# Kernel optimization log

Measured on AMD Instinct MI355X. Metric: run time of the kernel, lower is better.

The kernel has to match this reference:

```python
import jax, jax.numpy as jnp
import numpy as np
from jax import lax

WINDOW_SIZE = 11
SIGMA = 1.5
CHANNEL = 1
C1 = 0.01 ** 2
C2 = 0.03 ** 2
EPS = 1e-8


def _gaussian_window(window_size, sigma, channel):
    coords = jnp.arange(window_size, dtype=jnp.float32) - window_size // 2
    g = jnp.exp(-coords ** 2 / (2.0 * sigma ** 2))
    g = g / g.sum()
    w2d = jnp.outer(g, g)  # [ws, ws]
    # depthwise conv kernel, OIHW with I=1 (groups=channel)
    return jnp.broadcast_to(w2d[None, None], (channel, 1, window_size, window_size))


def _blur(x, window, channel):
    # depthwise 2D conv, SAME padding (padding = ws//2 for odd ws)
    return lax.conv_general_dilated(
        x, window, window_strides=(1, 1), padding="SAME",
        feature_group_count=channel,
        dimension_numbers=("NCHW", "OIHW", "NCHW"))


def setup_inputs() -> dict:
    key = jax.random.key(0)
    k1, k2 = jax.random.split(key)
    B, C, H, W = 32, CHANNEL, 512, 512
    pred = jax.random.uniform(k1, (B, C, H, W), dtype=jnp.float32)
    target = jax.random.uniform(k2, (B, C, H, W), dtype=jnp.float32)
    window = _gaussian_window(WINDOW_SIZE, SIGMA, CHANNEL)
    return {"pred": pred, "target": target, "window": window}


def reference(pred, target, window):
    channel = pred.shape[1]
    mu_p = _blur(pred, window, channel)
    mu_t = _blur(target, window, channel)
    mu_p_sq = mu_p ** 2
    mu_t_sq = mu_t ** 2
    mu_pt = mu_p * mu_t
    sigma_p_sq = _blur(pred ** 2, window, channel) - mu_p_sq
    sigma_t_sq = _blur(target ** 2, window, channel) - mu_t_sq
    sigma_pt = _blur(pred * target, window, channel) - mu_pt
    sigma_p_sq = jnp.maximum(sigma_p_sq, 0.0)
    sigma_t_sq = jnp.maximum(sigma_t_sq, 0.0)
    numerator = (2.0 * mu_pt + C1) * (2.0 * sigma_pt + C2)
    denominator = (mu_p_sq + mu_t_sq + C1) * (sigma_p_sq + sigma_t_sq + C2)
    ssim_map = numerator / (denominator + EPS)
    return 1.0 - jnp.mean(ssim_map)
```

## Files before the change

kernel.cpp:

```cpp
#include <hip/hip_runtime.h>

typedef short  s16x8 __attribute__((ext_vector_type(8)));
typedef unsigned short u16x8 __attribute__((ext_vector_type(8)));
typedef float  f32x4 __attribute__((ext_vector_type(4)));

#define B_   32
#define H_   512
#define W_   512
#define TX_  64
#define TY_  32
#define RX_  80
#define RYP_ 48
#define VXP_ 88
#define NBLK (B_ * (W_/TX_) * (H_/TY_))

__device__ __forceinline__ unsigned short f2bf(float x) {
    unsigned u = __builtin_bit_cast(unsigned, x);
    u += 0x7FFFu + ((u >> 16) & 1u);
    return (unsigned short)(u >> 16);
}

__global__ __launch_bounds__(256, 3)
void ssim_main(const float* __restrict__ pred,
               const float* __restrict__ targ,
               const float* __restrict__ win,
               float* __restrict__ partial)
{
    __shared__ __align__(16) unsigned short rawT[4][RX_][RYP_];
    __shared__ __align__(16) unsigned short vbuf[4][TY_][VXP_];
    __shared__ float gw[16];
    __shared__ float wsum[4];

    const int tid  = threadIdx.x;
    const int lane = tid & 63;
    const int wv   = tid >> 6;
    const int bid  = blockIdx.x;
    const int b    = bid >> 7;
    const int rem  = bid & 127;
    const int ty   = rem >> 3;
    const int tx   = rem & 7;
    const int x0g  = tx * TX_ - 5;
    const int y0g  = ty * TY_ - 5;

    if (tid < 11) {
        float s = 0.f;
        #pragma unroll
        for (int j = 0; j < 11; ++j) s += win[tid*11 + j];
        gw[tid] = s;
    }

    const float* pb = pred + (size_t)b * (H_*W_);
    const float* tb = targ + (size_t)b * (H_*W_);

    for (int idx = tid; idx < RX_ * 24; idx += 256) {
        const int x_l = idx % RX_;
        const int rp  = idx / RX_;
        const int gx  = x0g + x_l;
        const int gy0 = y0g + 2*rp;
        const bool xv = (unsigned)gx < (unsigned)W_;
        float p0=0.f, t0=0.f, p1=0.f, t1=0.f;
        if (xv && (unsigned)gy0 < (unsigned)H_) {
            const size_t o = (size_t)gy0 * W_ + gx; p0 = pb[o]; t0 = tb[o];
        }
        if (xv && (unsigned)(gy0+1) < (unsigned)H_) {
            const size_t o = (size_t)(gy0+1) * W_ + gx; p1 = pb[o]; t1 = tb[o];
        }
        const float s0 = fmaf(p0,p0, t0*t0), s1 = fmaf(p1,p1, t1*t1);
        const float q0 = p0*t0,              q1 = p1*t1;
        const int yo = 2*rp;
        *(unsigned*)&rawT[0][x_l][yo] = (unsigned)f2bf(p0) | ((unsigned)f2bf(p1) << 16);
        *(unsigned*)&rawT[1][x_l][yo] = (unsigned)f2bf(t0) | ((unsigned)f2bf(t1) << 16);
        *(unsigned*)&rawT[2][x_l][yo] = (unsigned)f2bf(s0) | ((unsigned)f2bf(s1) << 16);
        *(unsigned*)&rawT[3][x_l][yo] = (unsigned)f2bf(q0) | ((unsigned)f2bf(q1) << 16);
    }
    __syncthreads();

    const int mrow = lane & 15;
    const int quad = lane >> 4;
    s16x8 afr;
    #pragma unroll
    for (int j = 0; j < 8; ++j) {
        const int d = quad*8 + j - mrow;
        const float f = (d >= 0 && d < 11) ? gw[d] : 0.f;
        afr[j] = (short)f2bf(f);
    }
    const f32x4 zero4 = {0.f, 0.f, 0.f, 0.f};

    #pragma unroll
    for (int it = 0; it < 10; ++it) {
        const int X0c = (it >> 1) * 16;
        const int Yt  = (it & 1) * 16;
        const int xcol = X0c + mrow;
        const u16x8 braw = *(const u16x8*)&rawT[wv][xcol][Yt + quad*8];
        const s16x8 bfr  = __builtin_bit_cast(s16x8, braw);
        const f32x4 d = __builtin_amdgcn_mfma_f32_16x16x32_bf16(afr, bfr, zero4, 0, 0, 0);
        #pragma unroll
        for (int r = 0; r < 4; ++r)
            vbuf[wv][Yt + quad*4 + r][xcol] = f2bf(d[r]);
    }
    __syncthreads();

    float lsum = 0.f;
    const int X0 = wv * 16;
    #pragma unroll
    for (int yt = 0; yt < 2; ++yt) {
        const int Y0c = yt * 16;
        f32x4 dq[4];
        #pragma unroll
        for (int pl = 0; pl < 4; ++pl) {
            const u16x8 bv = *(const u16x8*)&vbuf[pl][Y0c + mrow][X0 + quad*8];
            const s16x8 bfr = __builtin_bit_cast(s16x8, bv);
            dq[pl] = __builtin_amdgcn_mfma_f32_16x16x32_bf16(afr, bfr, zero4, 0, 0, 0);
        }
        #pragma unroll
        for (int r = 0; r < 4; ++r) {
            const float mp = dq[0][r], mt = dq[1][r];
            const float sv = dq[2][r], qv = dq[3][r];
            const float mp2 = mp*mp, mt2 = mt*mt, mpt = mp*mt;
            const float sig = fmaxf(sv - mp2 - mt2, 0.f);
            const float cv  = qv - mpt;
            const float num = (2.f*mpt + 1e-4f) * (2.f*cv + 9e-4f);
            const float den = (mp2 + mt2 + 1e-4f) * (sig + 9e-4f);
            lsum += num * __builtin_amdgcn_rcpf(den + 1e-8f);
        }
    }

    #pragma unroll
    for (int off = 32; off > 0; off >>= 1)
        lsum += __shfl_down(lsum, off, 64);
    if (lane == 0) wsum[wv] = lsum;
    __syncthreads();
    if (tid == 0)
        partial[bid] = wsum[0] + wsum[1] + wsum[2] + wsum[3];
}

__global__ __launch_bounds__(256)
void ssim_reduce(const float* __restrict__ partial, float* __restrict__ out)
{
    __shared__ double ws[4];
    double s = 0.0;
    for (int i = threadIdx.x; i < NBLK; i += 256) s += (double)partial[i];
    #pragma unroll
    for (int off = 32; off > 0; off >>= 1)
        s += __shfl_down(s, off, 64);
    if ((threadIdx.x & 63) == 0) ws[threadIdx.x >> 6] = s;
    __syncthreads();
    if (threadIdx.x == 0) {
        const double tot = ws[0] + ws[1] + ws[2] + ws[3];
        const double n = (double)B_ * (double)H_ * (double)W_;
        out[0] = (float)(1.0 - tot / n);
    }
}

extern "C" void kernel_launch(void* const* d_in, const int* in_sizes, int n_in,
                              void* d_out, int out_size, void* d_ws, size_t ws_size,
                              hipStream_t stream)
{
    const float* pred = (const float*)d_in[0];
    const float* targ = (const float*)d_in[1];
    const float* win  = (const float*)d_in[2];
    float* out     = (float*)d_out;
    float* partial = (float*)d_ws;

    ssim_main<<<NBLK, 256, 0, stream>>>(pred, targ, win, partial);
    ssim_reduce<<<1, 256, 0, stream>>>(partial, out);
}
```

Before: 125.3 us.

## Fuse reduction into main kernel, use fp16 MFMA and smaller tiles

Reduces the output tile to 64x16 to double the block count and raise the occupancy target. Switches bf16 MFMA to fp16 with hardware packed conversion, and adds an XOR-swizzled LDS layout. Adds a branch-free interior load path. Replaces the separate reduction kernel with a last-block-done atomic counter to remove one launch. The trade-off is more halo reloading per output pixel and a persistent counter stored in the workspace.

```diff
diff --git a/kernel.cpp b/kernel.cpp
--- a/kernel.cpp
+++ b/kernel.cpp
@@ -1,125 +1,139 @@
 #include <hip/hip_runtime.h>
 
-typedef short  s16x8 __attribute__((ext_vector_type(8)));
-typedef unsigned short u16x8 __attribute__((ext_vector_type(8)));
-typedef float  f32x4 __attribute__((ext_vector_type(4)));
+typedef _Float16 f16x2 __attribute__((ext_vector_type(2)));
+typedef _Float16 f16x4 __attribute__((ext_vector_type(4)));
+typedef _Float16 f16x8 __attribute__((ext_vector_type(8)));
+typedef float    f32x4 __attribute__((ext_vector_type(4)));
 
-#define B_   32
-#define H_   512
-#define W_   512
-#define TX_  64
-#define TY_  32
-#define RX_  80
-#define RYP_ 48
-#define VXP_ 88
-#define NBLK (B_ * (W_/TX_) * (H_/TY_))
+#define NBLK 8192
 
-__device__ __forceinline__ unsigned short f2bf(float x) {
-    unsigned u = __builtin_bit_cast(unsigned, x);
-    u += 0x7FFFu + ((u >> 16) & 1u);
-    return (unsigned short)(u >> 16);
+__device__ __forceinline__ f16x2 pkrtz(float a, float b) {
+    return __builtin_bit_cast(f16x2, __builtin_amdgcn_cvt_pkrtz(a, b));
 }
 
-__global__ __launch_bounds__(256, 3)
-void ssim_main(const float* __restrict__ pred,
-               const float* __restrict__ targ,
-               const float* __restrict__ win,
-               float* __restrict__ partial)
+__global__ __launch_bounds__(256, 5)
+void ssim_fused(const float* __restrict__ pred,
+                const float* __restrict__ targ,
+                const float* __restrict__ win,
+                float* __restrict__ partial,
+                unsigned int* __restrict__ cnt,
+                float* __restrict__ out)
 {
-    __shared__ __align__(16) unsigned short rawT[4][RX_][RYP_];
-    __shared__ __align__(16) unsigned short vbuf[4][TY_][VXP_];
-    __shared__ float gw[16];
-    __shared__ float wsum[4];
+    __shared__ __align__(16) _Float16 rawT[4 * 80 * 32];
+    __shared__ __align__(16) _Float16 vbuf[4 * 16 * 88];
+    __shared__ float  gw[16];
+    __shared__ float  wsum[4];
+    __shared__ double dsum[4];
+    __shared__ int    go;
 
     const int tid  = threadIdx.x;
     const int lane = tid & 63;
     const int wv   = tid >> 6;
     const int bid  = blockIdx.x;
-    const int b    = bid >> 7;
-    const int rem  = bid & 127;
+    const int b    = bid >> 8;
+    const int rem  = bid & 255;
     const int ty   = rem >> 3;
     const int tx   = rem & 7;
-    const int x0g  = tx * TX_ - 5;
-    const int y0g  = ty * TY_ - 5;
+    const int x0g  = tx * 64 - 5;
+    const int y0g  = ty * 16 - 5;
 
     if (tid < 11) {
         float s = 0.f;
         #pragma unroll
-        for (int j = 0; j < 11; ++j) s += win[tid*11 + j];
+        for (int j = 0; j < 11; ++j) s += win[tid * 11 + j];
         gw[tid] = s;
     }
 
-    const float* pb = pred + (size_t)b * (H_*W_);
-    const float* tb = targ + (size_t)b * (H_*W_);
+    const float* pb = pred + (size_t)b * (512 * 512);
+    const float* tb = targ + (size_t)b * (512 * 512);
+    const bool interior = (tx >= 1) & (tx <= 6) & (ty >= 1) & (ty <= 30);
 
-    for (int idx = tid; idx < RX_ * 24; idx += 256) {
-        const int x_l = idx % RX_;
-        const int rp  = idx / RX_;
-        const int gx  = x0g + x_l;
-        const int gy0 = y0g + 2*rp;
-        const bool xv = (unsigned)gx < (unsigned)W_;
-        float p0=0.f, t0=0.f, p1=0.f, t1=0.f;
-        if (xv && (unsigned)gy0 < (unsigned)H_) {
-            const size_t o = (size_t)gy0 * W_ + gx; p0 = pb[o]; t0 = tb[o];
+    if (tid < 240) {
+        const int x  = tid % 80;
+        const int r0 = tid / 80;
+        const int gx = x0g + x;
+        const int sw = (x >> 1) & 7;
+        const bool xok = (unsigned)gx < 512u;
+        _Float16* rb = &rawT[x * 32];
+        for (int qy = r0; qy < 8; qy += 3) {
+            const int gy = y0g + qy * 4;
+            float p0, p1, p2, p3, t0, t1, t2, t3;
+            if (interior) {
+                const float* pp = pb + (size_t)gy * 512 + gx;
+                const float* tp = tb + (size_t)gy * 512 + gx;
+                p0 = pp[0]; p1 = pp[512]; p2 = pp[1024]; p3 = pp[1536];
+                t0 = tp[0]; t1 = tp[512]; t2 = tp[1024]; t3 = tp[1536];
+            } else {
+                p0 = p1 = p2 = p3 = t0 = t1 = t2 = t3 = 0.f;
+                if (xok) {
+                    const float* pp = pb + (size_t)gy * 512 + gx;
+                    const float* tp = tb + (size_t)gy * 512 + gx;
+                    if ((unsigned)(gy    ) < 512u) { p0 = pp[0];    t0 = tp[0];    }
+                    if ((unsigned)(gy + 1) < 512u) { p1 = pp[512];  t1 = tp[512];  }
+                    if ((unsigned)(gy + 2) < 512u) { p2 = pp[1024]; t2 = tp[1024]; }
+                    if ((unsigned)(gy + 3) < 512u) { p3 = pp[1536]; t3 = tp[1536]; }
+                }
+            }
+            const int off = (qy ^ sw) << 2;
+            union { f16x2 h2[2]; f16x4 v; } u;
+            u.h2[0] = pkrtz(p0, p1);
+            u.h2[1] = pkrtz(p2, p3);
+            *(f16x4*)&rb[off] = u.v;
+            u.h2[0] = pkrtz(t0, t1);
+            u.h2[1] = pkrtz(t2, t3);
+            *(f16x4*)&rb[2560 + off] = u.v;
+            u.h2[0] = pkrtz(fmaf(p0, p0, t0 * t0), fmaf(p1, p1, t1 * t1));
+            u.h2[1] = pkrtz(fmaf(p2, p2, t2 * t2), fmaf(p3, p3, t3 * t3));
+            *(f16x4*)&rb[5120 + off] = u.v;
+            u.h2[0] = pkrtz(p0 * t0, p1 * t1);
+            u.h2[1] = pkrtz(p2 * t2, p3 * t3);
+            *(f16x4*)&rb[7680 + off] = u.v;
         }
-        if (xv && (unsigned)(gy0+1) < (unsigned)H_) {
-            const size_t o = (size_t)(gy0+1) * W_ + gx; p1 = pb[o]; t1 = tb[o];
-        }
-        const float s0 = fmaf(p0,p0, t0*t0), s1 = fmaf(p1,p1, t1*t1);
-        const float q0 = p0*t0,              q1 = p1*t1;
-        const int yo = 2*rp;
-        *(unsigned*)&rawT[0][x_l][yo] = (unsigned)f2bf(p0) | ((unsigned)f2bf(p1) << 16);
-        *(unsigned*)&rawT[1][x_l][yo] = (unsigned)f2bf(t0) | ((unsigned)f2bf(t1) << 16);
-        *(unsigned*)&rawT[2][x_l][yo] = (unsigned)f2bf(s0) | ((unsigned)f2bf(s1) << 16);
-        *(unsigned*)&rawT[3][x_l][yo] = (unsigned)f2bf(q0) | ((unsigned)f2bf(q1) << 16);
     }
     __syncthreads();
 
     const int mrow = lane & 15;
     const int quad = lane >> 4;
-    s16x8 afr;
+    f16x8 afr;
     #pragma unroll
     for (int j = 0; j < 8; ++j) {
-        const int d = quad*8 + j - mrow;
-        const float f = (d >= 0 && d < 11) ? gw[d] : 0.f;
-        afr[j] = (short)f2bf(f);
+        const int d = quad * 8 + j - mrow;
+        afr[j] = (d >= 0 && d < 11) ? (_Float16)gw[d] : (_Float16)0.f;
     }
-    const f32x4 zero4 = {0.f, 0.f, 0.f, 0.f};
+    const f32x4 z4 = {0.f, 0.f, 0.f, 0.f};
 
+    const int swr = mrow >> 1;
     #pragma unroll
-    for (int it = 0; it < 10; ++it) {
-        const int X0c = (it >> 1) * 16;
-        const int Yt  = (it & 1) * 16;
-        const int xcol = X0c + mrow;
-        const u16x8 braw = *(const u16x8*)&rawT[wv][xcol][Yt + quad*8];
-        const s16x8 bfr  = __builtin_bit_cast(s16x8, braw);
-        const f32x4 d = __builtin_amdgcn_mfma_f32_16x16x32_bf16(afr, bfr, zero4, 0, 0, 0);
+    for (int c = 0; c < 5; ++c) {
+        const int x = c * 16 + mrow;
+        const _Float16* base = &rawT[wv * 2560 + x * 32];
+        union { f16x4 h[2]; f16x8 v; } bu;
+        bu.h[0] = *(const f16x4*)&base[((2 * quad    ) ^ swr) << 2];
+        bu.h[1] = *(const f16x4*)&base[((2 * quad + 1) ^ swr) << 2];
+        const f32x4 dv = __builtin_amdgcn_mfma_f32_16x16x32_f16(afr, bu.v, z4, 0, 0, 0);
         #pragma unroll
         for (int r = 0; r < 4; ++r)
-            vbuf[wv][Yt + quad*4 + r][xcol] = f2bf(d[r]);
+            vbuf[wv * 1408 + (quad * 4 + r) * 88 + x] = (_Float16)dv[r];
     }
     __syncthreads();
 
     float lsum = 0.f;
-    const int X0 = wv * 16;
-    #pragma unroll
-    for (int yt = 0; yt < 2; ++yt) {
-        const int Y0c = yt * 16;
+    {
+        const int X0 = wv * 16;
         f32x4 dq[4];
         #pragma unroll
         for (int pl = 0; pl < 4; ++pl) {
-            const u16x8 bv = *(const u16x8*)&vbuf[pl][Y0c + mrow][X0 + quad*8];
-            const s16x8 bfr = __builtin_bit_cast(s16x8, bv);
-            dq[pl] = __builtin_amdgcn_mfma_f32_16x16x32_bf16(afr, bfr, zero4, 0, 0, 0);
+            const f16x8 bv = *(const f16x8*)&vbuf[pl * 1408 + mrow * 88 + X0 + quad * 8];
+            dq[pl] = __builtin_amdgcn_mfma_f32_16x16x32_f16(afr, bv, z4, 0, 0, 0);
         }
         #pragma unroll
         for (int r = 0; r < 4; ++r) {
             const float mp = dq[0][r], mt = dq[1][r];
             const float sv = dq[2][r], qv = dq[3][r];
-            const float mp2 = mp*mp, mt2 = mt*mt, mpt = mp*mt;
+            const float mp2 = mp * mp, mt2 = mt * mt, mpt = mp * mt;
             const float sig = fmaxf(sv - mp2 - mt2, 0.f);
             const float cv  = qv - mpt;
-            const float num = (2.f*mpt + 1e-4f) * (2.f*cv + 9e-4f);
+            const float num = (2.f * mpt + 1e-4f) * (2.f * cv + 9e-4f);
             const float den = (mp2 + mt2 + 1e-4f) * (sig + 9e-4f);
             lsum += num * __builtin_amdgcn_rcpf(den + 1e-8f);
         }
@@ -130,25 +144,28 @@
         lsum += __shfl_down(lsum, off, 64);
     if (lane == 0) wsum[wv] = lsum;
     __syncthreads();
-    if (tid == 0)
-        partial[bid] = wsum[0] + wsum[1] + wsum[2] + wsum[3];
-}
-
-__global__ __launch_bounds__(256)
-void ssim_reduce(const float* __restrict__ partial, float* __restrict__ out)
-{
-    __shared__ double ws[4];
-    double s = 0.0;
-    for (int i = threadIdx.x; i < NBLK; i += 256) s += (double)partial[i];
-    #pragma unroll
-    for (int off = 32; off > 0; off >>= 1)
-        s += __shfl_down(s, off, 64);
-    if ((threadIdx.x & 63) == 0) ws[threadIdx.x >> 6] = s;
+    if (tid == 0) {
+        const float pblk = wsum[0] + wsum[1] + wsum[2] + wsum[3];
+        atomicExch(&partial[bid], pblk);
+        __threadfence();
+        const unsigned old = atomicAdd(cnt, 1u);
+        go = (((old + 1u) & (unsigned)(NBLK - 1)) == 0u);
+    }
     __syncthreads();
-    if (threadIdx.x == 0) {
-        const double tot = ws[0] + ws[1] + ws[2] + ws[3];
-        const double n = (double)B_ * (double)H_ * (double)W_;
-        out[0] = (float)(1.0 - tot / n);
+    if (go) {
+        __threadfence();
+        double s = 0.0;
+        for (int i = tid; i < NBLK; i += 256)
+            s += (double)atomicAdd(&partial[i], 0.0f);
+        #pragma unroll
+        for (int off = 32; off > 0; off >>= 1)
+            s += __shfl_down(s, off, 64);
+        if (lane == 0) dsum[wv] = s;
+        __syncthreads();
+        if (tid == 0) {
+            const double tot = dsum[0] + dsum[1] + dsum[2] + dsum[3];
+            out[0] = (float)(1.0 - tot / 8388608.0);
+        }
     }
 }
 
@@ -159,9 +176,9 @@
     const float* pred = (const float*)d_in[0];
     const float* targ = (const float*)d_in[1];
     const float* win  = (const float*)d_in[2];
-    float* out     = (float*)d_out;
-    float* partial = (float*)d_ws;
+    float* out = (float*)d_out;
+    float*        partial = (float*)d_ws;
+    unsigned int* cnt     = (unsigned int*)((char*)d_ws + NBLK * sizeof(float));
 
-    ssim_main<<<NBLK, 256, 0, stream>>>(pred, targ, win, partial);
-    ssim_reduce<<<1, 256, 0, stream>>>(partial, out);
+    ssim_fused<<<NBLK, 256, 0, stream>>>(pred, targ, win, partial, cnt, out);
 }
```

New measurement: 272.5 us. 2.17x slower.
